# Kernel tuning notes

Hardware: AMD Instinct MI355X
Metric: run time of the kernel (lower is better)

## Reference

```python
import jax, jax.numpy as jnp
import numpy as np

B, S, D = 1, 2048, 2048
H, KVH = 32, 8
HD = D // H          # 64
N_REP = H // KVH     # 4
ROPE_THETA = 10000.0
NEG = -1e9


def setup_inputs() -> dict:
    key = jax.random.key(0)
    ks = jax.random.split(key, 8)
    x = jax.random.normal(ks[0], (B, S, D), dtype=jnp.float32)
    # RoPE tables: freqs_cis[t, j] = exp(i * t * theta^{-2j/HD}), j in [0, HD/2)
    inv_freq = 1.0 / (ROPE_THETA ** (jnp.arange(0, HD, 2, dtype=jnp.float32) / HD))
    angles = jnp.arange(S, dtype=jnp.float32)[:, None] * inv_freq[None, :]  # (S, HD/2)
    freqs_cos = jnp.cos(angles)
    freqs_sin = jnp.sin(angles)
    # causal additive mask (S, S)
    mask = jnp.where(jnp.tril(jnp.ones((S, S), dtype=bool)), 0.0, NEG).astype(jnp.float32)
    sc = 0.02
    wq = jax.random.normal(ks[1], (D, H * HD), dtype=jnp.float32) * sc
    wk = jax.random.normal(ks[2], (D, KVH * HD), dtype=jnp.float32) * sc
    wv = jax.random.normal(ks[3], (D, KVH * HD), dtype=jnp.float32) * sc
    wo = jax.random.normal(ks[4], (H * HD, D), dtype=jnp.float32) * sc
    fw = jax.random.normal(ks[5], (HD, HD), dtype=jnp.float32) * sc
    fb = jnp.zeros((HD,), dtype=jnp.float32)
    return {"x": x, "freqs_cos": freqs_cos, "freqs_sin": freqs_sin, "mask": mask,
            "wq": wq, "wk": wk, "wv": wv, "wo": wo, "fw": fw, "fb": fb,
            "start_pos": 0}


def _rope(t, cos, sin):
    # t: (B, S, h, HD) -> complex rotate pairs along last dim
    tr = t.reshape(*t.shape[:-1], HD // 2, 2)
    c = cos[None, :, None, :]  # (1, S, 1, HD/2)
    s = sin[None, :, None, :]
    re = tr[..., 0] * c - tr[..., 1] * s
    im = tr[..., 0] * s + tr[..., 1] * c
    return jnp.stack([re, im], axis=-1).reshape(t.shape)


def reference(x, freqs_cos, freqs_sin, mask, wq, wk, wv, wo, fw, fb, start_pos):
    b, s, _ = x.shape
    xq = (x @ wq).reshape(b, s, H, HD)
    xk = (x @ wk).reshape(b, s, KVH, HD)
    xv = (x @ wv).reshape(b, s, KVH, HD)
    xq = _rope(xq, freqs_cos, freqs_sin)
    xk = _rope(xk, freqs_cos, freqs_sin)
    # GQA: repeat kv heads (repeat_interleave on head dim)
    keys = jnp.repeat(xk, N_REP, axis=2)    # (b, s, H, HD)
    values = jnp.repeat(xv, N_REP, axis=2)
    q = xq.transpose(0, 2, 1, 3)            # (b, H, s, HD)
    k = keys.transpose(0, 2, 1, 3)
    v = values.transpose(0, 2, 1, 3)
    scores = jnp.einsum("bhqd,bhkd->bhqk", q, k) / np.sqrt(HD).astype(np.float32)
    scores = scores + mask[None, None, :, :]
    probs = jax.nn.softmax(scores.astype(jnp.float32), axis=-1).astype(q.dtype)
    out = jnp.einsum("bhqk,bhkd->bhqd", probs, v)  # (b, H, s, HD)
    # shared per-head FFN: Linear(HD, HD) + SiLU, vectorized over heads
    out = jax.nn.silu(out @ fw + fb)
    out = out.transpose(0, 2, 1, 3).reshape(b, s, H * HD)
    return out @ wo
```

## Files before the change

kernel.cpp:

```cpp
#include <hip/hip_runtime.h>
#include <stdint.h>

#define S_LEN 2048
#define DMODEL 2048
#define NH 32
#define NKV 8
#define HD 64

typedef __attribute__((ext_vector_type(8))) __bf16 bf16x8;
typedef __attribute__((ext_vector_type(4))) float f32x4;
typedef __attribute__((ext_vector_type(16))) float f32x16;

__device__ __forceinline__ unsigned short f2bf(float f) {
    union { float f; uint32_t u; } v; v.f = f;
    uint32_t u = v.u;
    u += 0x7FFFu + ((u >> 16) & 1u);
    return (unsigned short)(u >> 16);
}

__device__ __forceinline__ uint32_t cvt_pk_bf16(float lo, float hi) {
    uint32_t r;
    asm("v_cvt_pk_bf16_f32 %0, %1, %2" : "=v"(r) : "v"(lo), "v"(hi));
    return r;
}

#define GLDS16(g, l)                                                          \
    __builtin_amdgcn_global_load_lds(                                         \
        (const __attribute__((address_space(1))) unsigned int*)(g),           \
        (__attribute__((address_space(3))) unsigned int*)(l), 16, 0, 0)

__device__ const int kUQT[24] = {15,15,7,14,14,13,13,6,12,12,11,11,5,10,10,9,9,4,8,8,3,2,1,0};
__device__ const int kUCH[24] = {0,1,0,0,1,0,1,0,0,1,0,1,0,0,1,0,1,0,0,1,0,0,0,0};
__device__ const int kUSP[24] = {1,1,0,1,1,1,1,0,1,1,1,1,0,1,1,1,1,0,1,1,0,0,0,0};

__global__ void cast_bf16_kernel(const float* __restrict__ src,
                                 unsigned short* __restrict__ dst, int n) {
    int g = (blockIdx.x * blockDim.x + threadIdx.x) * 8;
    if (g >= n) return;
    float4 a = *(const float4*)&src[g];
    float4 b = *(const float4*)&src[g + 4];
    unsigned short o[8];
    o[0] = f2bf(a.x); o[1] = f2bf(a.y); o[2] = f2bf(a.z); o[3] = f2bf(a.w);
    o[4] = f2bf(b.x); o[5] = f2bf(b.y); o[6] = f2bf(b.z); o[7] = f2bf(b.w);
    *(uint4*)&dst[g] = *(const uint4*)o;
}

__global__ void prep_transpose_kernel(
    const float* __restrict__ wq, const float* __restrict__ wk,
    const float* __restrict__ wv, const float* __restrict__ wo,
    const float* __restrict__ fw, unsigned short* __restrict__ wqkvT,
    unsigned short* __restrict__ woT, unsigned short* __restrict__ fwT) {
    __shared__ float tile[32][33];
    const int z = blockIdx.z;
    const float* src;
    unsigned short* dst;
    int R, C;
    if (z == 0)      { src = wq; dst = wqkvT;                         R = 2048; C = 2048; }
    else if (z == 1) { src = wk; dst = wqkvT + (size_t)2048 * 2048;   R = 2048; C = 512;  if (blockIdx.x >= 16) return; }
    else if (z == 2) { src = wv; dst = wqkvT + (size_t)2560 * 2048;   R = 2048; C = 512;  if (blockIdx.x >= 16) return; }
    else if (z == 3) { src = wo; dst = woT;                           R = 2048; C = 2048; }
    else             { src = fw; dst = fwT;                           R = 64;   C = 64;   if (blockIdx.x >= 2 || blockIdx.y >= 2) return; }
    int c0 = blockIdx.x * 32, r0 = blockIdx.y * 32;
    int tx = threadIdx.x, ty = threadIdx.y;
#pragma unroll
    for (int i = 0; i < 32; i += 8)
        tile[ty + i][tx] = src[(size_t)(r0 + ty + i) * C + c0 + tx];
    __syncthreads();
#pragma unroll
    for (int i = 0; i < 32; i += 8)
        dst[(size_t)(c0 + ty + i) * R + r0 + tx] = f2bf(tile[tx][ty + i]);
}

template <int MODE>
__global__ __launch_bounds__(256) void gemm_bt_kernel(
    const unsigned short* __restrict__ A, const unsigned short* __restrict__ BT,
    float* __restrict__ C0, unsigned short* __restrict__ Qb,
    unsigned short* __restrict__ Kb, unsigned short* __restrict__ VT,
    const float* __restrict__ fcos, const float* __restrict__ fsin,
    int M, int N, int K) {
    __shared__ unsigned short As[3][64 * 32];
    __shared__ unsigned short Bs[3][64 * 32];
    const int t = threadIdx.x;
    const int lane = t & 63, wave = t >> 6;
    const int wr = wave >> 1, wc = wave & 1;
    const int gx = gridDim.x;
    const int nwg = gx * gridDim.y;
    const int wg = blockIdx.y * gx + blockIdx.x;
    const int swz = (wg & 7) * (nwg >> 3) + (wg >> 3);
    const int m0 = (swz % gx) * 64, n0 = (swz / gx) * 64;
    const int l15 = lane & 15, lhi = lane >> 4;
    f32x4 acc[2][2] = {};
    const unsigned short* ga = A + (size_t)(m0 + (t >> 2)) * K + (t & 3) * 8;
    const unsigned short* gb = BT + (size_t)(n0 + (t >> 2)) * K + (t & 3) * 8;
    const int nk = K >> 5;

#define GSTAGE(buf, kt)                                                       \
    {                                                                         \
        const int k0_ = (kt) * 32;                                            \
        GLDS16(ga + k0_, &As[buf][t * 8]);                                    \
        GLDS16(gb + k0_, &Bs[buf][t * 8]);                                    \
    }

    GSTAGE(0, 0);
    GSTAGE(1, 1);

    int cb = 0, pfb = 2;
#pragma unroll 1
    for (int kt = 0; kt < nk; ++kt) {
        if (kt + 1 < nk) asm volatile("s_waitcnt vmcnt(2)" ::: "memory");
        else             asm volatile("s_waitcnt vmcnt(0)" ::: "memory");
        __builtin_amdgcn_s_barrier();
        __builtin_amdgcn_sched_barrier(0);
        if (kt + 2 < nk) GSTAGE(pfb, kt + 2);
        pfb = (pfb == 2) ? 0 : pfb + 1;
        const int mycb = cb;
        cb = (cb == 2) ? 0 : cb + 1;
        bf16x8 af[2], bfr[2];
#pragma unroll
        for (int m = 0; m < 2; m++)
            af[m] = *(const bf16x8*)&As[mycb][(wr * 32 + m * 16 + l15) * 32 + lhi * 8];
#pragma unroll
        for (int n = 0; n < 2; n++)
            bfr[n] = *(const bf16x8*)&Bs[mycb][(wc * 32 + n * 16 + l15) * 32 + lhi * 8];
#pragma unroll
        for (int m = 0; m < 2; m++)
#pragma unroll
            for (int n = 0; n < 2; n++)
                acc[m][n] = __builtin_amdgcn_mfma_f32_16x16x32_bf16(
                    af[m], bfr[n], acc[m][n], 0, 0, 0);
    }
#undef GSTAGE
    if (MODE == 0) {
#pragma unroll
        for (int m = 0; m < 2; m++) {
            int row = m0 + wr * 32 + m * 16 + lhi * 4;
#pragma unroll
            for (int n = 0; n < 2; n++) {
                int col = n0 + wc * 32 + n * 16 + l15;
#pragma unroll
                for (int r = 0; r < 4; r++)
                    C0[(size_t)(row + r) * N + col] = acc[m][n][r];
            }
        }
    } else {
        const int nblk = n0 >> 6;
        if (nblk < 40) {
            const float CS = 0.125f * 1.44269504f;
            const bool isQ = (nblk < 32);
            unsigned short* dst = isQ ? Qb + (size_t)nblk * (S_LEN * HD)
                                      : Kb + (size_t)(nblk - 32) * (S_LEN * HD);
#pragma unroll
            for (int m = 0; m < 2; m++) {
#pragma unroll
                for (int n = 0; n < 2; n++) {
                    int col = wc * 32 + n * 16 + l15;
                    int i = col >> 1;
                    float sgn = (col & 1) ? 1.f : -1.f;
#pragma unroll
                    for (int r = 0; r < 4; r++) {
                        int s = m0 + wr * 32 + m * 16 + lhi * 4 + r;
                        float c = fcos[s * 32 + i], sn = fsin[s * 32 + i];
                        float v = acc[m][n][r];
                        float pv = __shfl_xor(v, 1);
                        float o = fmaf(pv, sgn * sn, v * c);
                        if (isQ) o *= CS;
                        dst[(size_t)s * HD + col] = f2bf(o);
                    }
                }
            }
        } else {
            const int kvh = nblk - 40;
            unsigned short* ldsT = (unsigned short*)As;
            __syncthreads();
#pragma unroll
            for (int m = 0; m < 2; m++)
#pragma unroll
                for (int n = 0; n < 2; n++) {
                    int d = wc * 32 + n * 16 + l15;
#pragma unroll
                    for (int r = 0; r < 4; r++) {
                        int sl = wr * 32 + m * 16 + lhi * 4 + r;
                        ldsT[d * 66 + sl] = f2bf(acc[m][n][r]);
                    }
                }
            __syncthreads();
            const int d = t >> 2, sc = (t & 3) * 16;
            unsigned short* dst = VT + ((size_t)kvh * HD + d) * S_LEN + m0 + sc;
            const unsigned short* srcl = &ldsT[d * 66 + sc];
#pragma unroll
            for (int j = 0; j < 8; j++)
                ((uint32_t*)dst)[j] = *(const uint32_t*)&srcl[2 * j];
        }
    }
}

__global__ __launch_bounds__(256) void flash_kernel(
    const unsigned short* __restrict__ Q, const unsigned short* __restrict__ Kg,
    const unsigned short* __restrict__ VTg, unsigned short* __restrict__ O,
    float* __restrict__ Opart, float* __restrict__ ML) {
    __shared__ unsigned short Ks[3][4096];
    __shared__ unsigned short Vs[3][4096];
    const int t = threadIdx.x, lane = t & 63, wave = t >> 6;
    const int l31 = lane & 31, hi = lane >> 5;
    const int bid = blockIdx.x;
    const int h = bid & 31, u = bid >> 5;
    const int qt = kUQT[u], ch = kUCH[u], sp = kUSP[u];
    const int kvh = h >> 2;

    const int kt0 = sp ? ch * (qt + 1) : 0;
    const int ktN = sp ? kt0 + qt + 1 : 2 * qt + 2;

    const int srow = t >> 3;
    const int scol = ((t & 7) * 8) ^ ((srow & 7) * 8);
    const unsigned short* gk = Kg + ((size_t)kvh * S_LEN + srow) * HD + scol;
    const unsigned short* gv = VTg + ((size_t)kvh * HD + srow) * S_LEN + scol;

    const int q0 = qt * 128;
    const int qw0 = q0 + wave * 32;
    const int q = qw0 + l31;

    const unsigned short* qp = Q + ((size_t)h * S_LEN + q) * HD + hi * 8;
    bf16x8 qf0 = *(const bf16x8*)(qp);
    bf16x8 qf1 = *(const bf16x8*)(qp + 16);
    bf16x8 qf2 = *(const bf16x8*)(qp + 32);
    bf16x8 qf3 = *(const bf16x8*)(qp + 48);

    f32x16 oacc0 = {}, oacc1 = {};
    float mrun = -1e30f, lrun = 0.f;

    {
        const size_t kva = (size_t)kt0 * 64, kvb = kva + 64;
        GLDS16(gk + kva * HD, &Ks[0][t * 8]);
        GLDS16(gk + (kva + 32) * HD, &Ks[0][t * 8 + 2048]);
        GLDS16(gv + kva, &Vs[0][t * 8]);
        GLDS16(gv + (size_t)32 * S_LEN + kva, &Vs[0][t * 8 + 2048]);
        GLDS16(gk + kvb * HD, &Ks[1][t * 8]);
        GLDS16(gk + (kvb + 32) * HD, &Ks[1][t * 8 + 2048]);
        GLDS16(gv + kvb, &Vs[1][t * 8]);
        GLDS16(gv + (size_t)32 * S_LEN + kvb, &Vs[1][t * 8 + 2048]);
    }

    int cb = 0, pfb = 2;
#pragma unroll 1
    for (int kt = kt0; kt < ktN; ++kt) {
        if (kt + 1 < ktN) asm volatile("s_waitcnt vmcnt(4)" ::: "memory");
        else              asm volatile("s_waitcnt vmcnt(0)" ::: "memory");
        __builtin_amdgcn_s_barrier();
        __builtin_amdgcn_sched_barrier(0);
        if (kt + 2 < ktN) {
            const size_t kvp = (size_t)(kt + 2) * 64;
            GLDS16(gk + kvp * HD, &Ks[pfb][t * 8]);
            GLDS16(gk + (kvp + 32) * HD, &Ks[pfb][t * 8 + 2048]);
            GLDS16(gv + kvp, &Vs[pfb][t * 8]);
            GLDS16(gv + (size_t)32 * S_LEN + kvp, &Vs[pfb][t * 8 + 2048]);
        }
        pfb = (pfb == 2) ? 0 : pfb + 1;
        const int kv0 = kt * 64;
        const int mycb = cb;
        cb = (cb == 2) ? 0 : cb + 1;
        if (kv0 > qw0 + 31) continue;
        const unsigned short* ksb = Ks[mycb];
        const unsigned short* vsb = Vs[mycb];
        const int sw = (l31 & 7) * 8;
        f32x16 s0 = {}, s1 = {};
#pragma unroll
        for (int kc = 0; kc < 4; kc++) {
            bf16x8 k0 = *(const bf16x8*)&ksb[l31 * 64 + ((16 * kc + 8 * hi) ^ sw)];
            bf16x8 k1 = *(const bf16x8*)&ksb[(32 + l31) * 64 + ((16 * kc + 8 * hi) ^ sw)];
            bf16x8 qc = (kc == 0) ? qf0 : (kc == 1) ? qf1 : (kc == 2) ? qf2 : qf3;
            s0 = __builtin_amdgcn_mfma_f32_32x32x16_bf16(k0, qc, s0, 0, 0, 0);
            s1 = __builtin_amdgcn_mfma_f32_32x32x16_bf16(k1, qc, s1, 0, 0, 0);
        }
        float p0[16], p1[16];
        if (kv0 + 63 <= qw0) {
#pragma unroll
            for (int r = 0; r < 16; r++) { p0[r] = s0[r]; p1[r] = s1[r]; }
        } else {
#pragma unroll
            for (int r = 0; r < 16; r++) {
                int rr = (r & 3) + 8 * (r >> 2) + 4 * hi;
                p0[r] = (kv0 + rr <= q) ? s0[r] : -1e30f;
                p1[r] = (kv0 + 32 + rr <= q) ? s1[r] : -1e30f;
            }
        }
        float t8[8];
#pragma unroll
        for (int r = 0; r < 8; r++)
            t8[r] = fmaxf(fmaxf(p0[r], p0[r + 8]), fmaxf(p1[r], p1[r + 8]));
        float lm = fmaxf(fmaxf(fmaxf(t8[0], t8[4]), fmaxf(t8[1], t8[5])),
                         fmaxf(fmaxf(t8[2], t8[6]), fmaxf(t8[3], t8[7])));
        if (!__all(lm - mrun <= 8.f)) {
            float rm = fmaxf(lm, __shfl_xor(lm, 32));
            float mnew = fmaxf(mrun, rm);
            float sc = exp2f(mrun - mnew);
            mrun = mnew;
            lrun *= sc;
            oacc0 *= sc;
            oacc1 *= sc;
        }
#pragma unroll
        for (int r = 0; r < 16; r++) {
            p0[r] = exp2f(p0[r] - mrun);
            p1[r] = exp2f(p1[r] - mrun);
        }
        float sA = 0.f, sB = 0.f, sC = 0.f, sD = 0.f;
#pragma unroll
        for (int r = 0; r < 4; r++) {
            sA += p0[r] + p1[r];
            sB += p0[r + 4] + p1[r + 4];
            sC += p0[r + 8] + p1[r + 8];
            sD += p0[r + 12] + p1[r + 12];
        }
        lrun += (sA + sB) + (sC + sD);
        bf16x8 pf[4];
#pragma unroll
        for (int kc = 0; kc < 4; kc++) {
            const int sub = (kc & 1) * 8;
            uint32_t Wl0, Wl1, Wh0, Wh1;
            if (kc < 2) {
                Wl0 = cvt_pk_bf16(p0[sub + 0], p0[sub + 1]);
                Wl1 = cvt_pk_bf16(p0[sub + 2], p0[sub + 3]);
                Wh0 = cvt_pk_bf16(p0[sub + 4], p0[sub + 5]);
                Wh1 = cvt_pk_bf16(p0[sub + 6], p0[sub + 7]);
            } else {
                Wl0 = cvt_pk_bf16(p1[sub + 0], p1[sub + 1]);
                Wl1 = cvt_pk_bf16(p1[sub + 2], p1[sub + 3]);
                Wh0 = cvt_pk_bf16(p1[sub + 4], p1[sub + 5]);
                Wh1 = cvt_pk_bf16(p1[sub + 6], p1[sub + 7]);
            }
            uint32_t sw0 = hi ? Wl0 : Wh0, sw1 = hi ? Wl1 : Wh1;
            uint32_t rc0 = __shfl_xor((int)sw0, 32);
            uint32_t rc1 = __shfl_xor((int)sw1, 32);
            uint32_t kp0 = hi ? Wh0 : Wl0, kp1 = hi ? Wh1 : Wl1;
            uint32_t F0 = hi ? rc0 : kp0;
            uint32_t F1 = hi ? rc1 : kp1;
            uint32_t F2 = hi ? kp0 : rc0;
            uint32_t F3 = hi ? kp1 : rc1;
            uint4 fu = {F0, F1, F2, F3};
            pf[kc] = *(const bf16x8*)&fu;
        }
#pragma unroll
        for (int kc = 0; kc < 4; kc++) {
            bf16x8 v0 = *(const bf16x8*)&vsb[l31 * 64 + ((16 * kc + 8 * hi) ^ sw)];
            bf16x8 v1 = *(const bf16x8*)&vsb[(32 + l31) * 64 + ((16 * kc + 8 * hi) ^ sw)];
            oacc0 = __builtin_amdgcn_mfma_f32_32x32x16_bf16(v0, pf[kc], oacc0, 0, 0, 0);
            oacc1 = __builtin_amdgcn_mfma_f32_32x32x16_bf16(v1, pf[kc], oacc1, 0, 0, 0);
        }
    }
    lrun += __shfl_xor(lrun, 32);
    const int qrow = wave * 32 + l31;
    if (sp) {
        const int pidx = (h * 8 + (qt - 8)) * 2 + ch;
        float* po = Opart + ((size_t)pidx * 128 + qrow) * 64 + 4 * hi;
#pragma unroll
        for (int g = 0; g < 4; g++) {
            float4 a = {oacc0[4 * g], oacc0[4 * g + 1], oacc0[4 * g + 2], oacc0[4 * g + 3]};
            *(float4*)(po + 8 * g) = a;
            float4 b = {oacc1[4 * g], oacc1[4 * g + 1], oacc1[4 * g + 2], oacc1[4 * g + 3]};
            *(float4*)(po + 32 + 8 * g) = b;
        }
        if (hi == 0) {
            ML[((size_t)pidx * 128 + qrow) * 2] = mrun;
            ML[((size_t)pidx * 128 + qrow) * 2 + 1] = lrun;
        }
    } else {
        float rinv = 1.f / lrun;
        unsigned short* ob = O + ((size_t)h * S_LEN + q) * HD + 4 * hi;
#pragma unroll
        for (int g = 0; g < 4; g++) {
            uint32_t a0 = cvt_pk_bf16(oacc0[4 * g] * rinv, oacc0[4 * g + 1] * rinv);
            uint32_t a1 = cvt_pk_bf16(oacc0[4 * g + 2] * rinv, oacc0[4 * g + 3] * rinv);
            uint2 u0 = {a0, a1};
            *(uint2*)(ob + 8 * g) = u0;
            uint32_t b0 = cvt_pk_bf16(oacc1[4 * g] * rinv, oacc1[4 * g + 1] * rinv);
            uint32_t b1 = cvt_pk_bf16(oacc1[4 * g + 2] * rinv, oacc1[4 * g + 3] * rinv);
            uint2 u1 = {b0, b1};
            *(uint2*)(ob + 32 + 8 * g) = u1;
        }
    }
}

__global__ __launch_bounds__(256) void flash_combine_kernel(
    const float* __restrict__ Opart, const float* __restrict__ ML,
    unsigned short* __restrict__ attn) {
    const int bid = blockIdx.x;
    const int h = bid & 31, j = bid >> 5;
    const int qt = 8 + j;
    const int t = threadIdx.x;
    const int qrow = t >> 1, d0 = (t & 1) * 32;
    const int base = (h * 8 + j) * 2;
    const float mA = ML[((size_t)base * 128 + qrow) * 2];
    const float lA = ML[((size_t)base * 128 + qrow) * 2 + 1];
    const float mB = ML[((size_t)(base + 1) * 128 + qrow) * 2];
    const float lB = ML[((size_t)(base + 1) * 128 + qrow) * 2 + 1];
    const float m = fmaxf(mA, mB);
    const float wA = exp2f(mA - m), wB = exp2f(mB - m);
    const float rinv = 1.f / (lA * wA + lB * wB);
    const float* pA = Opart + ((size_t)base * 128 + qrow) * 64 + d0;
    const float* pB = Opart + ((size_t)(base + 1) * 128 + qrow) * 64 + d0;
    unsigned short* po = attn + ((size_t)h * S_LEN + qt * 128 + qrow) * HD + d0;
#pragma unroll
    for (int dd = 0; dd < 32; dd += 8) {
        float4 a0 = *(const float4*)&pA[dd], a1 = *(const float4*)&pA[dd + 4];
        float4 b0 = *(const float4*)&pB[dd], b1 = *(const float4*)&pB[dd + 4];
        unsigned short o[8];
        o[0] = f2bf((a0.x * wA + b0.x * wB) * rinv);
        o[1] = f2bf((a0.y * wA + b0.y * wB) * rinv);
        o[2] = f2bf((a0.z * wA + b0.z * wB) * rinv);
        o[3] = f2bf((a0.w * wA + b0.w * wB) * rinv);
        o[4] = f2bf((a1.x * wA + b1.x * wB) * rinv);
        o[5] = f2bf((a1.y * wA + b1.y * wB) * rinv);
        o[6] = f2bf((a1.z * wA + b1.z * wB) * rinv);
        o[7] = f2bf((a1.w * wA + b1.w * wB) * rinv);
        *(uint4*)&po[dd] = *(const uint4*)o;
    }
}

__global__ __launch_bounds__(256) void fw_silu_kernel(
    const unsigned short* __restrict__ AT, const unsigned short* __restrict__ fwT,
    const float* __restrict__ fb, unsigned short* __restrict__ h2) {
    const int t = threadIdx.x, lane = t & 63, wave = t >> 6;
    const int l15 = lane & 15, lhi = lane >> 4;
    const int r0 = blockIdx.x * 64 + wave * 16;
    const unsigned short* ap = AT + (size_t)(r0 + l15) * HD + lhi * 8;
    bf16x8 a0 = *(const bf16x8*)ap;
    bf16x8 a1 = *(const bf16x8*)(ap + 32);
    f32x4 acc[4] = {};
#pragma unroll
    for (int nb = 0; nb < 4; nb++) {
        const unsigned short* bp = fwT + (size_t)(nb * 16 + l15) * HD + lhi * 8;
        bf16x8 b0 = *(const bf16x8*)bp;
        bf16x8 b1 = *(const bf16x8*)(bp + 32);
        acc[nb] = __builtin_amdgcn_mfma_f32_16x16x32_bf16(a0, b0, acc[nb], 0, 0, 0);
        acc[nb] = __builtin_amdgcn_mfma_f32_16x16x32_bf16(a1, b1, acc[nb], 0, 0, 0);
    }
#pragma unroll
    for (int nb = 0; nb < 4; nb++) {
        int col = nb * 16 + l15;
        float bias = fb[col];
#pragma unroll
        for (int r = 0; r < 4; r++) {
            int row = r0 + lhi * 4 + r;
            int s = row & (S_LEN - 1), hh = row >> 11;
            float x = acc[nb][r] + bias;
            float sg = 1.f / (1.f + exp2f(-x * 1.44269504f));
            h2[(size_t)s * DMODEL + hh * HD + col] = f2bf(x * sg);
        }
    }
}

extern "C" void kernel_launch(void* const* d_in, const int* in_sizes, int n_in,
                              void* d_out, int out_size, void* d_ws, size_t ws_size,
                              hipStream_t stream) {
    const float* x = (const float*)d_in[0];
    const float* fcos = (const float*)d_in[1];
    const float* fsin = (const float*)d_in[2];
    const float* wq = (const float*)d_in[4];
    const float* wk = (const float*)d_in[5];
    const float* wv = (const float*)d_in[6];
    const float* wo = (const float*)d_in[7];
    const float* fw = (const float*)d_in[8];
    const float* fb = (const float*)d_in[9];
    float* out = (float*)d_out;

    char* ws = (char*)d_ws;
    size_t off = 0;
    auto alloc = [&](size_t bytes) {
        void* p = ws + off;
        off += (bytes + 255) & ~(size_t)255;
        return p;
    };
    unsigned short* wqkvT = (unsigned short*)alloc((size_t)3072 * 2048 * 2);
    unsigned short* woT   = (unsigned short*)alloc((size_t)2048 * 2048 * 2);
    unsigned short* fwT   = (unsigned short*)alloc((size_t)64 * 64 * 2);
    unsigned short* Qb    = (unsigned short*)alloc((size_t)NH * S_LEN * HD * 2);
    unsigned short* Kb    = (unsigned short*)alloc((size_t)NKV * S_LEN * HD * 2);
    unsigned short* VT    = (unsigned short*)alloc((size_t)NKV * HD * S_LEN * 2);
    unsigned short* xb    = (unsigned short*)alloc((size_t)2048 * 2048 * 2);
    float*          ML    = (float*)alloc((size_t)512 * 128 * 2 * 4);
    unsigned short* attn  = (unsigned short*)alloc((size_t)NH * S_LEN * HD * 2);
    float*          Opart = (float*)alloc((size_t)512 * 128 * 64 * 4);
    unsigned short* h2 = xb;

    cast_bf16_kernel<<<2048, 256, 0, stream>>>(x, xb, 2048 * 2048);
    prep_transpose_kernel<<<dim3(64, 64, 5), dim3(32, 8), 0, stream>>>(
        wq, wk, wv, wo, fw, wqkvT, woT, fwT);

    gemm_bt_kernel<1><<<dim3(32, 48), 256, 0, stream>>>(
        xb, wqkvT, nullptr, Qb, Kb, VT, fcos, fsin, 2048, 3072, 2048);

    flash_kernel<<<768, 256, 0, stream>>>(Qb, Kb, VT, attn, Opart, ML);
    flash_combine_kernel<<<256, 256, 0, stream>>>(Opart, ML, attn);

    fw_silu_kernel<<<1024, 256, 0, stream>>>(attn, fwT, fb, h2);

    gemm_bt_kernel<0><<<dim3(32, 32), 256, 0, stream>>>(
        h2, woT, out, nullptr, nullptr, nullptr, nullptr, nullptr,
        2048, 2048, 2048);
}
```

Baseline: 170.5 us.

## Fuse prep kernels, merge split-KV combine into FFN, widen GEMM K-tile with swizzle

Folds the x-to-bf16 cast into the weight-transpose prep kernel as an extra grid slice, and packs transpose stores into 2-element writes. Removes the separate flash_combine kernel by having fw_silu merge the two split-KV partials for rows in the second half of the sequence. Doubles the GEMM K tile to 64 with an XOR-swizzled LDS layout to reduce bank conflicts and halve the number of barrier iterations. In exchange LDS use per block doubles, which may lower occupancy, and the FFN kernel does more uneven work per wave.

```diff
diff --git a/kernel.cpp b/kernel.cpp
--- a/kernel.cpp
+++ b/kernel.cpp
@@ -33,42 +33,46 @@
 __device__ const int kUCH[24] = {0,1,0,0,1,0,1,0,0,1,0,1,0,0,1,0,1,0,0,1,0,0,0,0};
 __device__ const int kUSP[24] = {1,1,0,1,1,1,1,0,1,1,1,1,0,1,1,1,1,0,1,1,0,0,0,0};
 
-__global__ void cast_bf16_kernel(const float* __restrict__ src,
-                                 unsigned short* __restrict__ dst, int n) {
-    int g = (blockIdx.x * blockDim.x + threadIdx.x) * 8;
-    if (g >= n) return;
-    float4 a = *(const float4*)&src[g];
-    float4 b = *(const float4*)&src[g + 4];
-    unsigned short o[8];
-    o[0] = f2bf(a.x); o[1] = f2bf(a.y); o[2] = f2bf(a.z); o[3] = f2bf(a.w);
-    o[4] = f2bf(b.x); o[5] = f2bf(b.y); o[6] = f2bf(b.z); o[7] = f2bf(b.w);
-    *(uint4*)&dst[g] = *(const uint4*)o;
-}
-
-__global__ void prep_transpose_kernel(
+__global__ void prep_kernel(
     const float* __restrict__ wq, const float* __restrict__ wk,
     const float* __restrict__ wv, const float* __restrict__ wo,
-    const float* __restrict__ fw, unsigned short* __restrict__ wqkvT,
-    unsigned short* __restrict__ woT, unsigned short* __restrict__ fwT) {
+    const float* __restrict__ fw, const float* __restrict__ x,
+    unsigned short* __restrict__ wqkvT, unsigned short* __restrict__ woT,
+    unsigned short* __restrict__ fwT, unsigned short* __restrict__ xb) {
+    const int z = blockIdx.z;
+    const int tx = threadIdx.x, ty = threadIdx.y;
+    if (z == 5) {
+        int base = (blockIdx.y * 64 + blockIdx.x) * 1024 + (ty * 32 + tx) * 4;
+        float4 a = *(const float4*)&x[base];
+        ushort4 o;
+        o.x = f2bf(a.x); o.y = f2bf(a.y); o.z = f2bf(a.z); o.w = f2bf(a.w);
+        *(ushort4*)&xb[base] = o;
+        return;
+    }
     __shared__ float tile[32][33];
-    const int z = blockIdx.z;
     const float* src;
     unsigned short* dst;
     int R, C;
-    if (z == 0)      { src = wq; dst = wqkvT;                         R = 2048; C = 2048; }
-    else if (z == 1) { src = wk; dst = wqkvT + (size_t)2048 * 2048;   R = 2048; C = 512;  if (blockIdx.x >= 16) return; }
-    else if (z == 2) { src = wv; dst = wqkvT + (size_t)2560 * 2048;   R = 2048; C = 512;  if (blockIdx.x >= 16) return; }
-    else if (z == 3) { src = wo; dst = woT;                           R = 2048; C = 2048; }
-    else             { src = fw; dst = fwT;                           R = 64;   C = 64;   if (blockIdx.x >= 2 || blockIdx.y >= 2) return; }
+    if (z == 0)      { src = wq; dst = wqkvT;                       R = 2048; C = 2048; }
+    else if (z == 1) { src = wk; dst = wqkvT + (size_t)2048 * 2048; R = 2048; C = 512;  if (blockIdx.x >= 16) return; }
+    else if (z == 2) { src = wv; dst = wqkvT + (size_t)2560 * 2048; R = 2048; C = 512;  if (blockIdx.x >= 16) return; }
+    else if (z == 3) { src = wo; dst = woT;                         R = 2048; C = 2048; }
+    else             { src = fw; dst = fwT;                         R = 64;   C = 64;   if (blockIdx.x >= 2 || blockIdx.y >= 2) return; }
     int c0 = blockIdx.x * 32, r0 = blockIdx.y * 32;
-    int tx = threadIdx.x, ty = threadIdx.y;
 #pragma unroll
     for (int i = 0; i < 32; i += 8)
         tile[ty + i][tx] = src[(size_t)(r0 + ty + i) * C + c0 + tx];
     __syncthreads();
-#pragma unroll
-    for (int i = 0; i < 32; i += 8)
-        dst[(size_t)(c0 + ty + i) * R + r0 + tx] = f2bf(tile[tx][ty + i]);
+    const int tid = ty * 32 + tx;
+#pragma unroll
+    for (int it = 0; it < 2; ++it) {
+        int idx = tid + it * 256;
+        int c = idx >> 4, rp = idx & 15;
+        ushort2 o;
+        o.x = f2bf(tile[2 * rp][c]);
+        o.y = f2bf(tile[2 * rp + 1][c]);
+        *(ushort2*)&dst[(size_t)(c0 + c) * R + r0 + 2 * rp] = o;
+    }
 }
 
 template <int MODE>
@@ -78,8 +82,8 @@
     unsigned short* __restrict__ Kb, unsigned short* __restrict__ VT,
     const float* __restrict__ fcos, const float* __restrict__ fsin,
     int M, int N, int K) {
-    __shared__ unsigned short As[3][64 * 32];
-    __shared__ unsigned short Bs[3][64 * 32];
+    __shared__ unsigned short As[3][64 * 64];
+    __shared__ unsigned short Bs[3][64 * 64];
     const int t = threadIdx.x;
     const int lane = t & 63, wave = t >> 6;
     const int wr = wave >> 1, wc = wave & 1;
@@ -90,15 +94,20 @@
     const int m0 = (swz % gx) * 64, n0 = (swz / gx) * 64;
     const int l15 = lane & 15, lhi = lane >> 4;
     f32x4 acc[2][2] = {};
-    const unsigned short* ga = A + (size_t)(m0 + (t >> 2)) * K + (t & 3) * 8;
-    const unsigned short* gb = BT + (size_t)(n0 + (t >> 2)) * K + (t & 3) * 8;
-    const int nk = K >> 5;
+    const int srow = t >> 3;
+    const int sslot = (t & 7) ^ (srow & 7);
+    const unsigned short* ga = A + (size_t)(m0 + srow) * K + sslot * 8;
+    const unsigned short* gb = BT + (size_t)(n0 + srow) * K + sslot * 8;
+    const int nk = K >> 6;
+    const int rsw = (l15 & 7) << 3;
 
 #define GSTAGE(buf, kt)                                                       \
     {                                                                         \
-        const int k0_ = (kt) * 32;                                            \
+        const int k0_ = (kt) * 64;                                            \
         GLDS16(ga + k0_, &As[buf][t * 8]);                                    \
+        GLDS16(ga + (size_t)32 * K + k0_, &As[buf][t * 8 + 2048]);            \
         GLDS16(gb + k0_, &Bs[buf][t * 8]);                                    \
+        GLDS16(gb + (size_t)32 * K + k0_, &Bs[buf][t * 8 + 2048]);            \
     }
 
     GSTAGE(0, 0);
@@ -107,7 +116,7 @@
     int cb = 0, pfb = 2;
 #pragma unroll 1
     for (int kt = 0; kt < nk; ++kt) {
-        if (kt + 1 < nk) asm volatile("s_waitcnt vmcnt(2)" ::: "memory");
+        if (kt + 1 < nk) asm volatile("s_waitcnt vmcnt(4)" ::: "memory");
         else             asm volatile("s_waitcnt vmcnt(0)" ::: "memory");
         __builtin_amdgcn_s_barrier();
         __builtin_amdgcn_sched_barrier(0);
@@ -115,19 +124,27 @@
         pfb = (pfb == 2) ? 0 : pfb + 1;
         const int mycb = cb;
         cb = (cb == 2) ? 0 : cb + 1;
-        bf16x8 af[2], bfr[2];
+        bf16x8 af[2][2], bfr[2][2];
 #pragma unroll
         for (int m = 0; m < 2; m++)
-            af[m] = *(const bf16x8*)&As[mycb][(wr * 32 + m * 16 + l15) * 32 + lhi * 8];
+#pragma unroll
+            for (int kc = 0; kc < 2; kc++)
+                af[m][kc] = *(const bf16x8*)&As[mycb][
+                    ((wr * 32 + m * 16 + l15) * 64 + kc * 32 + lhi * 8) ^ rsw];
 #pragma unroll
         for (int n = 0; n < 2; n++)
-            bfr[n] = *(const bf16x8*)&Bs[mycb][(wc * 32 + n * 16 + l15) * 32 + lhi * 8];
-#pragma unroll
-        for (int m = 0; m < 2; m++)
-#pragma unroll
-            for (int n = 0; n < 2; n++)
-                acc[m][n] = __builtin_amdgcn_mfma_f32_16x16x32_bf16(
-                    af[m], bfr[n], acc[m][n], 0, 0, 0);
+#pragma unroll
+            for (int kc = 0; kc < 2; kc++)
+                bfr[n][kc] = *(const bf16x8*)&Bs[mycb][
+                    ((wc * 32 + n * 16 + l15) * 64 + kc * 32 + lhi * 8) ^ rsw];
+#pragma unroll
+        for (int kc = 0; kc < 2; kc++)
+#pragma unroll
+            for (int m = 0; m < 2; m++)
+#pragma unroll
+                for (int n = 0; n < 2; n++)
+                    acc[m][n] = __builtin_amdgcn_mfma_f32_16x16x32_bf16(
+                        af[m][kc], bfr[n][kc], acc[m][n], 0, 0, 0);
     }
 #undef GSTAGE
     if (MODE == 0) {
@@ -380,51 +397,45 @@
     }
 }
 
-__global__ __launch_bounds__(256) void flash_combine_kernel(
-    const float* __restrict__ Opart, const float* __restrict__ ML,
-    unsigned short* __restrict__ attn) {
-    const int bid = blockIdx.x;
-    const int h = bid & 31, j = bid >> 5;
-    const int qt = 8 + j;
-    const int t = threadIdx.x;
-    const int qrow = t >> 1, d0 = (t & 1) * 32;
-    const int base = (h * 8 + j) * 2;
-    const float mA = ML[((size_t)base * 128 + qrow) * 2];
-    const float lA = ML[((size_t)base * 128 + qrow) * 2 + 1];
-    const float mB = ML[((size_t)(base + 1) * 128 + qrow) * 2];
-    const float lB = ML[((size_t)(base + 1) * 128 + qrow) * 2 + 1];
-    const float m = fmaxf(mA, mB);
-    const float wA = exp2f(mA - m), wB = exp2f(mB - m);
-    const float rinv = 1.f / (lA * wA + lB * wB);
-    const float* pA = Opart + ((size_t)base * 128 + qrow) * 64 + d0;
-    const float* pB = Opart + ((size_t)(base + 1) * 128 + qrow) * 64 + d0;
-    unsigned short* po = attn + ((size_t)h * S_LEN + qt * 128 + qrow) * HD + d0;
-#pragma unroll
-    for (int dd = 0; dd < 32; dd += 8) {
-        float4 a0 = *(const float4*)&pA[dd], a1 = *(const float4*)&pA[dd + 4];
-        float4 b0 = *(const float4*)&pB[dd], b1 = *(const float4*)&pB[dd + 4];
-        unsigned short o[8];
-        o[0] = f2bf((a0.x * wA + b0.x * wB) * rinv);
-        o[1] = f2bf((a0.y * wA + b0.y * wB) * rinv);
-        o[2] = f2bf((a0.z * wA + b0.z * wB) * rinv);
-        o[3] = f2bf((a0.w * wA + b0.w * wB) * rinv);
-        o[4] = f2bf((a1.x * wA + b1.x * wB) * rinv);
-        o[5] = f2bf((a1.y * wA + b1.y * wB) * rinv);
-        o[6] = f2bf((a1.z * wA + b1.z * wB) * rinv);
-        o[7] = f2bf((a1.w * wA + b1.w * wB) * rinv);
-        *(uint4*)&po[dd] = *(const uint4*)o;
-    }
-}
-
 __global__ __launch_bounds__(256) void fw_silu_kernel(
     const unsigned short* __restrict__ AT, const unsigned short* __restrict__ fwT,
-    const float* __restrict__ fb, unsigned short* __restrict__ h2) {
+    const float* __restrict__ fb, const float* __restrict__ Opart,
+    const float* __restrict__ ML, unsigned short* __restrict__ h2) {
     const int t = threadIdx.x, lane = t & 63, wave = t >> 6;
     const int l15 = lane & 15, lhi = lane >> 4;
     const int r0 = blockIdx.x * 64 + wave * 16;
-    const unsigned short* ap = AT + (size_t)(r0 + l15) * HD + lhi * 8;
-    bf16x8 a0 = *(const bf16x8*)ap;
-    bf16x8 a1 = *(const bf16x8*)(ap + 32);
+    const int row = r0 + l15;
+    const int hh = row >> 11, s = row & (S_LEN - 1);
+    bf16x8 a0, a1;
+    if (s < 1024) {
+        const unsigned short* ap = AT + (size_t)row * HD + lhi * 8;
+        a0 = *(const bf16x8*)ap;
+        a1 = *(const bf16x8*)(ap + 32);
+    } else {
+        const int qt = s >> 7, qrow = s & 127;
+        const int pidx = (hh * 8 + (qt - 8)) * 2;
+        const float* mlp = ML + ((size_t)pidx * 128 + qrow) * 2;
+        const float* mlq = ML + ((size_t)(pidx + 1) * 128 + qrow) * 2;
+        float mA = mlp[0], lA = mlp[1], mB = mlq[0], lB = mlq[1];
+        float mm = fmaxf(mA, mB);
+        float wA = exp2f(mA - mm), wB = exp2f(mB - mm);
+        float rv = 1.f / (lA * wA + lB * wB);
+        const float* pA = Opart + ((size_t)pidx * 128 + qrow) * 64;
+        const float* pB = pA + 8192;
+#pragma unroll
+        for (int half = 0; half < 2; half++) {
+            int db = half * 32 + lhi * 8;
+            float4 x0 = *(const float4*)&pA[db], x1 = *(const float4*)&pA[db + 4];
+            float4 y0 = *(const float4*)&pB[db], y1 = *(const float4*)&pB[db + 4];
+            uint32_t w0 = cvt_pk_bf16((x0.x * wA + y0.x * wB) * rv, (x0.y * wA + y0.y * wB) * rv);
+            uint32_t w1 = cvt_pk_bf16((x0.z * wA + y0.z * wB) * rv, (x0.w * wA + y0.w * wB) * rv);
+            uint32_t w2 = cvt_pk_bf16((x1.x * wA + y1.x * wB) * rv, (x1.y * wA + y1.y * wB) * rv);
+            uint32_t w3 = cvt_pk_bf16((x1.z * wA + y1.z * wB) * rv, (x1.w * wA + y1.w * wB) * rv);
+            uint4 u = {w0, w1, w2, w3};
+            if (half == 0) a0 = *(const bf16x8*)&u;
+            else           a1 = *(const bf16x8*)&u;
+        }
+    }
     f32x4 acc[4] = {};
 #pragma unroll
     for (int nb = 0; nb < 4; nb++) {
@@ -440,11 +451,11 @@
         float bias = fb[col];
 #pragma unroll
         for (int r = 0; r < 4; r++) {
-            int row = r0 + lhi * 4 + r;
-            int s = row & (S_LEN - 1), hh = row >> 11;
-            float x = acc[nb][r] + bias;
-            float sg = 1.f / (1.f + exp2f(-x * 1.44269504f));
-            h2[(size_t)s * DMODEL + hh * HD + col] = f2bf(x * sg);
+            int orow = r0 + lhi * 4 + r;
+            int os = orow & (S_LEN - 1), oh = orow >> 11;
+            float xv = acc[nb][r] + bias;
+            float sg = 1.f / (1.f + exp2f(-xv * 1.44269504f));
+            h2[(size_t)os * DMODEL + oh * HD + col] = f2bf(xv * sg);
         }
     }
 }
@@ -482,17 +493,15 @@
     float*          Opart = (float*)alloc((size_t)512 * 128 * 64 * 4);
     unsigned short* h2 = xb;
 
-    cast_bf16_kernel<<<2048, 256, 0, stream>>>(x, xb, 2048 * 2048);
-    prep_transpose_kernel<<<dim3(64, 64, 5), dim3(32, 8), 0, stream>>>(
-        wq, wk, wv, wo, fw, wqkvT, woT, fwT);
+    prep_kernel<<<dim3(64, 64, 6), dim3(32, 8), 0, stream>>>(
+        wq, wk, wv, wo, fw, x, wqkvT, woT, fwT, xb);
 
     gemm_bt_kernel<1><<<dim3(32, 48), 256, 0, stream>>>(
         xb, wqkvT, nullptr, Qb, Kb, VT, fcos, fsin, 2048, 3072, 2048);
 
     flash_kernel<<<768, 256, 0, stream>>>(Qb, Kb, VT, attn, Opart, ML);
-    flash_combine_kernel<<<256, 256, 0, stream>>>(Opart, ML, attn);
-
-    fw_silu_kernel<<<1024, 256, 0, stream>>>(attn, fwT, fb, h2);
+
+    fw_silu_kernel<<<1024, 256, 0, stream>>>(attn, fwT, fb, Opart, ML, h2);
 
     gemm_bt_kernel<0><<<dim3(32, 32), 256, 0, stream>>>(
         h2, woT, out, nullptr, nullptr, nullptr, nullptr, nullptr,
```

Measured after the change: 175.6 us. 1.03x slower.
